# Performance work log

Measured on AMD Instinct MI355X. Metric: run time of the kernel, lower is better.

## Reference

```python
import jax, jax.numpy as jnp
import numpy as np

EMBED_DIM = 768
NUM_HEADS = 12
HEAD_DIM = EMBED_DIM // NUM_HEADS
SCALE = HEAD_DIM ** -0.5
LN_EPS = 1e-5


def layer_norm(x, gamma, beta):
    mu = jnp.mean(x, axis=-1, keepdims=True)
    var = jnp.var(x, axis=-1, keepdims=True)
    return (x - mu) * jax.lax.rsqrt(var + LN_EPS) * gamma + beta


def setup_inputs() -> dict:
    key = jax.random.key(0)
    ks = jax.random.split(key, 10)
    B, N, M, C = 4, 4096, 256, EMBED_DIM
    inp = {
        "input_tokens": jax.random.normal(ks[0], (B, N, C), dtype=jnp.float32),
        "query_tokens": jax.random.normal(ks[1], (B, M, C), dtype=jnp.float32),
        "Wq": jax.random.normal(ks[2], (C, C), dtype=jnp.float32) * 0.02,
        "bq": jnp.zeros((C,), dtype=jnp.float32),
        "Wk": jax.random.normal(ks[3], (C, C), dtype=jnp.float32) * 0.02,
        "bk": jnp.zeros((C,), dtype=jnp.float32),
        "Wv": jax.random.normal(ks[4], (C, C), dtype=jnp.float32) * 0.02,
        "bv": jnp.zeros((C,), dtype=jnp.float32),
        "gq_ln": jnp.ones((C,), dtype=jnp.float32),
        "bq_ln": jnp.zeros((C,), dtype=jnp.float32),
        "gk_ln": jnp.ones((C,), dtype=jnp.float32),
        "bk_ln": jnp.zeros((C,), dtype=jnp.float32),
    }
    return inp


def reference(input_tokens, query_tokens, Wq, bq, Wk, bk, Wv, bv,
              gq_ln, bq_ln, gk_ln, bk_ln):
    B, N, C = input_tokens.shape
    _, M, _ = query_tokens.shape
    H, D = NUM_HEADS, HEAD_DIM

    # v: Linear only (no LayerNorm on the attn=None path)
    v = (input_tokens @ Wv.T + bv).reshape(B, N, H, D).transpose(0, 2, 1, 3)   # [B,H,N,D]
    # q, k: Linear -> LayerNorm over full embed_dim, then split heads
    q = layer_norm(query_tokens @ Wq.T + bq, gq_ln, bq_ln)
    q = q.reshape(B, M, H, D).transpose(0, 2, 1, 3) * SCALE                    # [B,H,M,D]
    k = layer_norm(input_tokens @ Wk.T + bk, gk_ln, bk_ln)
    k = k.reshape(B, N, H, D).transpose(0, 2, 1, 3)                            # [B,H,N,D]

    attn = jax.nn.softmax(jnp.einsum('bhmd,bhnd->bhmn', q, k), axis=-1)        # [B,H,M,N]
    out = jnp.einsum('bhmn,bhnd->bhmd', attn, v)                               # [B,H,M,D]
    out = out.transpose(0, 2, 1, 3).reshape(B, M, C)
    return (query_tokens + out, attn)
```

## Files before the change

kernel.cpp:

```cpp
#include <hip/hip_runtime.h>
#include <math.h>

#define BB 4
#define NN 4096
#define MM 256
#define CC 768
#define HH 12
#define DD 64
#define SCALEF 0.125f
#define LN_EPSF 1e-5f

typedef __attribute__((ext_vector_type(4))) float f32x4;
typedef __attribute__((ext_vector_type(16))) float f32x16;
typedef __attribute__((ext_vector_type(8))) _Float16 f16x8;
typedef __attribute__((ext_vector_type(4))) _Float16 f16x4;

__device__ __forceinline__ void gldh(const _Float16* g, _Float16* l) {
    __builtin_amdgcn_global_load_lds(
        (const __attribute__((address_space(1))) void*)g,
        (__attribute__((address_space(3))) void*)l, 16, 0, 0);
}

__global__ __launch_bounds__(256) void conv_all(
    const float* __restrict__ x0, _Float16* __restrict__ y0, long long n0,
    const float* __restrict__ x1, _Float16* __restrict__ y1, long long n1,
    const float* __restrict__ x2, _Float16* __restrict__ y2, long long n2,
    const float* __restrict__ x3, _Float16* __restrict__ y3, long long n3,
    const float* __restrict__ x4, _Float16* __restrict__ y4, long long n4)
{
    long long i = ((long long)blockIdx.x * 256 + threadIdx.x) * 8;
    const long long total = n0 + n1 + n2 + n3 + n4;
    const long long stride = (long long)gridDim.x * 256 * 8;
    for (; i < total; i += stride) {
        const float* x; _Float16* y; long long off = i;
        if (off < n0) { x = x0; y = y0; }
        else if ((off -= n0) < n1) { x = x1; y = y1; }
        else if ((off -= n1) < n2) { x = x2; y = y2; }
        else if ((off -= n2) < n3) { x = x3; y = y3; }
        else { off -= n3; x = x4; y = y4; }
        float4 a = *(const float4*)(x + off);
        float4 b = *(const float4*)(x + off + 4);
        f16x8 o;
        o[0] = (_Float16)a.x; o[1] = (_Float16)a.y;
        o[2] = (_Float16)a.z; o[3] = (_Float16)a.w;
        o[4] = (_Float16)b.x; o[5] = (_Float16)b.y;
        o[6] = (_Float16)b.z; o[7] = (_Float16)b.w;
        *(f16x8*)(y + off) = o;
    }
}

__global__ __launch_bounds__(256) void proj_kv_f16(
    const _Float16* __restrict__ Xh,
    const _Float16* __restrict__ X2h,
    const _Float16* __restrict__ Wkh, const _Float16* __restrict__ Wqh,
    const _Float16* __restrict__ Wvh,
    const float* __restrict__ bk, const float* __restrict__ bq,
    const float* __restrict__ bv,
    _Float16* __restrict__ Klin, _Float16* __restrict__ Qlin,
    _Float16* __restrict__ Vth)
{
    __shared__ _Float16 As[2][4096];
    __shared__ _Float16 Bks[2][4096];
    __shared__ _Float16 Bvs[2][4096];

    const int bid = blockIdx.x;
    const _Float16* Ag; const _Float16* Bkg;
    const float* biask; _Float16* outk;
    bool hasV;
    int bm, bn;
    if (bid < 768) {
        bm = bid & 127; bn = bid >> 7;
        Ag = Xh; Bkg = Wkh; biask = bk; outk = Klin; hasV = true;
    } else {
        const int sid = bid - 768;
        bm = sid & 7; bn = sid >> 3;
        Ag = X2h; Bkg = Wqh; biask = bq; outk = Qlin; hasV = false;
    }
    const int row0 = bm * 128, col0 = bn * 128;

    const int tid = threadIdx.x;
    const int w = tid >> 6, lane = tid & 63;
    const int wr = w >> 1, wc = w & 1;
    const int fr = lane & 15, kg = lane >> 4;

    f32x4 acck[4][4], accv[4][4];
#pragma unroll
    for (int m = 0; m < 4; ++m)
#pragma unroll
        for (int n = 0; n < 4; ++n) {
            acck[m][n] = (f32x4){0.f, 0.f, 0.f, 0.f};
            accv[m][n] = (f32x4){0.f, 0.f, 0.f, 0.f};
        }

#define STAGE(sel, kt)                                                           \
    do {                                                                         \
        const int kk = (kt) << 5;                                                \
        _Pragma("unroll")                                                        \
        for (int i = 0; i < 2; ++i) {                                            \
            const int cbase = (i * 4 + w) * 64;                                  \
            const int c = cbase + lane;                                          \
            const int row = c >> 2, ks = (c & 3) << 3;                           \
            gldh(Ag  + (size_t)(row0 + row) * CC + kk + ks, &As[sel][cbase * 8]);\
            gldh(Bkg + (size_t)(col0 + row) * CC + kk + ks, &Bks[sel][cbase * 8]);\
            gldh(Wvh + (size_t)(col0 + row) * CC + kk + ks, &Bvs[sel][cbase * 8]);\
        }                                                                        \
    } while (0)

    STAGE(0, 0);
    int cur = 0;
    const int nk = CC >> 5;
    for (int kt = 0; kt < nk; ++kt) {
        __syncthreads();
        if (kt + 1 < nk) STAGE(cur ^ 1, kt + 1);
        const _Float16* lA = As[cur];
        const _Float16* lBk = Bks[cur];
        const _Float16* lBv = Bvs[cur];
        f16x8 a[4];
#pragma unroll
        for (int m = 0; m < 4; ++m)
            a[m] = *(const f16x8*)(lA + (wr * 64 + m * 16 + fr) * 32 + kg * 8);
#pragma unroll
        for (int n = 0; n < 4; ++n) {
            f16x8 bkf = *(const f16x8*)(lBk + (wc * 64 + n * 16 + fr) * 32 + kg * 8);
            __builtin_amdgcn_s_setprio(1);
#pragma unroll
            for (int m = 0; m < 4; ++m)
                acck[m][n] = __builtin_amdgcn_mfma_f32_16x16x32_f16(
                    a[m], bkf, acck[m][n], 0, 0, 0);
            __builtin_amdgcn_s_setprio(0);
            f16x8 bvf = *(const f16x8*)(lBv + (wc * 64 + n * 16 + fr) * 32 + kg * 8);
            __builtin_amdgcn_s_setprio(1);
#pragma unroll
            for (int m = 0; m < 4; ++m)
                accv[m][n] = __builtin_amdgcn_mfma_f32_16x16x32_f16(
                    a[m], bvf, accv[m][n], 0, 0, 0);
            __builtin_amdgcn_s_setprio(0);
        }
        cur ^= 1;
    }
#undef STAGE

    {
        float bvv[4];
#pragma unroll
        for (int n = 0; n < 4; ++n)
            bvv[n] = biask[col0 + wc * 64 + n * 16 + fr];
#pragma unroll
        for (int m = 0; m < 4; ++m)
#pragma unroll
            for (int n = 0; n < 4; ++n) {
                const int col = col0 + wc * 64 + n * 16 + fr;
#pragma unroll
                for (int r = 0; r < 4; ++r) {
                    const int row = row0 + wr * 64 + m * 16 + kg * 4 + r;
                    outk[(size_t)row * CC + col] = (_Float16)(acck[m][n][r] + bvv[n]);
                }
            }
    }
    if (hasV) {
        const int b = row0 >> 12;
        const int rb = row0 & 4095;
#pragma unroll
        for (int n = 0; n < 4; ++n) {
            const int cg = col0 + wc * 64 + n * 16 + fr;
            const int hh = cg >> 6, d = cg & 63;
            const float bb = bv[cg];
            _Float16* vrow = Vth + ((size_t)((b * HH + hh) * DD + d)) * NN + rb + wr * 64;
#pragma unroll
            for (int m = 0; m < 4; ++m) {
                f16x4 v4;
#pragma unroll
                for (int r = 0; r < 4; ++r)
                    v4[r] = (_Float16)(accv[m][n][r] + bb);
                *(f16x4*)(vrow + m * 16 + kg * 4) = v4;
            }
        }
    }
}

__global__ __launch_bounds__(256) void ln_rows_f16(
    const _Float16* __restrict__ Y, _Float16* __restrict__ outh,
    const float* __restrict__ g, const float* __restrict__ be, const float scale)
{
    const int row = blockIdx.x;
    const _Float16* y = Y + (size_t)row * CC;
    const int tid = threadIdx.x;
    float x0 = (float)y[tid], x1 = (float)y[tid + 256], x2 = (float)y[tid + 512];
    float s = x0 + x1 + x2;
    float q = x0 * x0 + x1 * x1 + x2 * x2;
#pragma unroll
    for (int o = 32; o >= 1; o >>= 1) {
        s += __shfl_xor(s, o, 64);
        q += __shfl_xor(q, o, 64);
    }
    __shared__ float sh_s[4], sh_q[4];
    const int w = tid >> 6;
    if ((tid & 63) == 0) { sh_s[w] = s; sh_q[w] = q; }
    __syncthreads();
    s = sh_s[0] + sh_s[1] + sh_s[2] + sh_s[3];
    q = sh_q[0] + sh_q[1] + sh_q[2] + sh_q[3];
    const float mu  = s * (1.f / 768.f);
    const float var = q * (1.f / 768.f) - mu * mu;
    const float inv = rsqrtf(var + LN_EPSF);
    _Float16* o = outh + (size_t)row * CC;
    o[tid]       = (_Float16)(((x0 - mu) * inv * g[tid]       + be[tid])       * scale);
    o[tid + 256] = (_Float16)(((x1 - mu) * inv * g[tid + 256] + be[tid + 256]) * scale);
    o[tid + 512] = (_Float16)(((x2 - mu) * inv * g[tid + 512] + be[tid + 512]) * scale);
}

__global__ __launch_bounds__(256, 4) void attn_stats(
    const _Float16* __restrict__ Qh,
    const _Float16* __restrict__ Kh,
    float* __restrict__ stats)
{
    __shared__ __align__(16) unsigned char smem[37888];
    _Float16* Kl = (_Float16*)smem;
    _Float16* Ql = (_Float16*)(smem + 32768);
    float (*red)[32][2] = (float(*)[32][2])(smem + 36864);

    const int tid = threadIdx.x;
    const int w = tid >> 6, lane = tid & 63;
    const int l5 = lane >> 5, lm = lane & 31;
    const int bid = blockIdx.x;
    const int mt = bid / 192;
    const int rem = bid % 192;
    const int bh = rem >> 2, ns = rem & 3;
    const int h = bh % HH, b = bh / HH;
    const int qr0 = mt * 32;
    const int nb = ns * 1024;

#define STAGEK(sel, c0)                                                         \
    _Pragma("unroll")                                                           \
    for (int i = 0; i < 4; ++i) {                                               \
        const int L = i * 256 + tid;                                            \
        const int n = L >> 3, pos = L & 7;                                      \
        gldh(Kh + (size_t)(b * NN + (c0) + n) * CC + h * DD + ((pos ^ (n & 7)) << 3), \
             &Kl[(sel) * 8192 + (i * 256 + w * 64) * 8]);                       \
    }

    {
        const int n = tid >> 3, pos = tid & 7;
        gldh(Qh + (size_t)(b * MM + qr0 + n) * CC + h * DD + ((pos ^ (n & 7)) << 3),
             &Ql[(w * 64) * 8]);
    }
    STAGEK(0, nb);
    __syncthreads();
    f16x8 qf[4];
#pragma unroll
    for (int ks = 0; ks < 4; ++ks)
        qf[ks] = *(const f16x8*)&Ql[lm * 64 + (((ks * 2 + l5) ^ (lm & 7)) << 3)];

    const int nl = w * 32 + lm;

    float mrun = -1e30f, srun = 0.f;
    int cur = 0;
    for (int c = 0; c < 8; ++c) {
        if (c) __syncthreads();
        if (c + 1 < 8) STAGEK(cur ^ 1, nb + (c + 1) * 128);
        const _Float16* Kb = Kl + cur * 8192;
        f32x16 s;
#pragma unroll
        for (int r = 0; r < 16; ++r) s[r] = 0.f;
        __builtin_amdgcn_s_setprio(1);
#pragma unroll
        for (int ks = 0; ks < 4; ++ks) {
            f16x8 kf = *(const f16x8*)&Kb[nl * 64 + (((ks * 2 + l5) ^ (nl & 7)) << 3)];
            s = __builtin_amdgcn_mfma_f32_32x32x16_f16(kf, qf[ks], s, 0, 0, 0);
        }
        __builtin_amdgcn_s_setprio(0);
        float cmax = s[0];
#pragma unroll
        for (int r = 1; r < 16; ++r) cmax = fmaxf(cmax, s[r]);
        cmax = fmaxf(cmax, __shfl_xor(cmax, 32, 64));
        const float nm = fmaxf(mrun, cmax);
        float cs = 0.f;
#pragma unroll
        for (int r = 0; r < 16; ++r) cs += __expf(s[r] - nm);
        cs += __shfl_xor(cs, 32, 64);
        srun = srun * __expf(mrun - nm) + cs;
        mrun = nm;
        cur ^= 1;
    }
    if (lane < 32) { red[w][lane][0] = mrun; red[w][lane][1] = srun; }
    __syncthreads();
    if (w == 0 && lane < 32) {
        float M = -1e30f;
#pragma unroll
        for (int ww = 0; ww < 4; ++ww) M = fmaxf(M, red[ww][lane][0]);
        float S = 0.f;
#pragma unroll
        for (int ww = 0; ww < 4; ++ww) S += red[ww][lane][1] * __expf(red[ww][lane][0] - M);
        float* sp = stats + ((size_t)((bh * 8 + mt) * 32 + lane)) * 8 + ns * 2;
        sp[0] = M; sp[1] = S;
    }
#undef STAGEK
}

__global__ __launch_bounds__(256, 2) void attn_main(
    const _Float16* __restrict__ Qh, const _Float16* __restrict__ Kh,
    const _Float16* __restrict__ Vt,
    const float* __restrict__ stats, const float* __restrict__ qtok,
    float* __restrict__ attn, float* __restrict__ out0)
{
    __shared__ __align__(16) unsigned char smem[77824];
    _Float16* Kl = (_Float16*)smem;
    _Float16* Vl = (_Float16*)(smem + 32768);
    _Float16* Ql = (_Float16*)(smem + 65536);
    _Float16* Pl = (_Float16*)(smem + 69632);
    float* rbuf = (float*)smem;

    const int tid = threadIdx.x;
    const int w = tid >> 6, lane = tid & 63;
    const int l5 = lane >> 5, lm = lane & 31;
    const int bh = blockIdx.x % 48;
    const int mt = blockIdx.x / 48;
    const int h = bh % HH, b = bh / HH;
    const int qr0 = mt * 32;

#define STAGEK(sel, c0)                                                         \
    _Pragma("unroll")                                                           \
    for (int i = 0; i < 4; ++i) {                                               \
        const int L = i * 256 + tid;                                            \
        const int n = L >> 3, pos = L & 7;                                      \
        gldh(Kh + (size_t)(b * NN + (c0) + n) * CC + h * DD + ((pos ^ (n & 7)) << 3), \
             &Kl[(sel) * 8192 + (i * 256 + w * 64) * 8]);                       \
    }
#define STAGEV(sel, c0)                                                         \
    _Pragma("unroll")                                                           \
    for (int i = 0; i < 4; ++i) {                                               \
        const int L = i * 256 + tid;                                            \
        const int d = L >> 4, pos = L & 15;                                     \
        const int blk = (pos & 8) | ((pos & 7) ^ (d & 7));                      \
        gldh(Vt + (size_t)(bh * DD + d) * NN + (c0) + blk * 8,                  \
             &Vl[(sel) * 8192 + (i * 256 + w * 64) * 8]);                       \
    }

    float M, invS;
    {
        const float* sp = stats + ((size_t)((bh * 8 + mt) * 32 + lm)) * 8;
        M = -1e30f;
#pragma unroll
        for (int n2 = 0; n2 < 4; ++n2) M = fmaxf(M, sp[n2 * 2]);
        float S = 0.f;
#pragma unroll
        for (int n2 = 0; n2 < 4; ++n2) S += sp[n2 * 2 + 1] * __expf(sp[n2 * 2] - M);
        invS = 1.f / S;
    }

    {
        const int n = tid >> 3, pos = tid & 7;
        gldh(Qh + (size_t)(b * MM + qr0 + n) * CC + h * DD + ((pos ^ (n & 7)) << 3),
             &Ql[(w * 64) * 8]);
    }
    STAGEK(0, 0); STAGEV(0, 0);
    __syncthreads();
    f16x8 qf[4];
#pragma unroll
    for (int ks = 0; ks < 4; ++ks)
        qf[ks] = *(const f16x8*)&Ql[lm * 64 + (((ks * 2 + l5) ^ (lm & 7)) << 3)];

    const int nl = w * 32 + lm;

    f32x16 oacc[2];
#pragma unroll
    for (int dt = 0; dt < 2; ++dt)
#pragma unroll
        for (int r = 0; r < 16; ++r) oacc[dt][r] = 0.f;

    float* attnRow = attn + ((size_t)(bh * MM + qr0 + lm)) * NN;

    int cur = 0;
    for (int c = 0; c < 32; ++c) {
        if (c) {
            asm volatile("s_waitcnt vmcnt(4)" ::: "memory");
            __builtin_amdgcn_s_barrier();
            __builtin_amdgcn_sched_barrier(0);
        }
        if (c + 1 < 32) { STAGEK(cur ^ 1, (c + 1) * 128); STAGEV(cur ^ 1, (c + 1) * 128); }
        __builtin_amdgcn_sched_barrier(0);
        const _Float16* Kb = Kl + cur * 8192;
        const _Float16* Vb = Vl + cur * 8192;
        f32x16 s;
#pragma unroll
        for (int r = 0; r < 16; ++r) s[r] = 0.f;
        __builtin_amdgcn_s_setprio(1);
#pragma unroll
        for (int ks = 0; ks < 4; ++ks) {
            f16x8 kf = *(const f16x8*)&Kb[nl * 64 + (((ks * 2 + l5) ^ (nl & 7)) << 3)];
            s = __builtin_amdgcn_mfma_f32_32x32x16_f16(kf, qf[ks], s, 0, 0, 0);
        }
        __builtin_amdgcn_s_setprio(0);
#pragma unroll
        for (int q = 0; q < 4; ++q) {
            float4 pw;
            f16x4 ph;
#pragma unroll
            for (int r = 0; r < 4; ++r) {
                const float p = __expf(s[q * 4 + r] - M) * invS;
                ((float*)&pw)[r] = p;
                ph[r] = (_Float16)p;
            }
            *(float4*)(attnRow + c * 128 + w * 32 + q * 8 + l5 * 4) = pw;
            const int blk16 = w * 4 + q;
            const int pos = (blk16 & 8) | ((blk16 & 7) ^ (lm & 7));
            *(f16x4*)&Pl[lm * 128 + pos * 8 + l5 * 4] = ph;
        }
        __builtin_amdgcn_s_setprio(1);
#pragma unroll
        for (int ks = 0; ks < 2; ++ks) {
            const int blk16 = w * 4 + ks * 2 + l5;
            const int posP = (blk16 & 8) | ((blk16 & 7) ^ (lm & 7));
            f16x8 pf = *(const f16x8*)&Pl[lm * 128 + posP * 8];
#pragma unroll
            for (int dt = 0; dt < 2; ++dt) {
                const int d = dt * 32 + lm;
                const int posV = (blk16 & 8) | ((blk16 & 7) ^ (d & 7));
                f16x8 vf = *(const f16x8*)&Vb[d * 128 + posV * 8];
                oacc[dt] = __builtin_amdgcn_mfma_f32_32x32x16_f16(pf, vf, oacc[dt], 0, 0, 0);
            }
        }
        __builtin_amdgcn_s_setprio(0);
        cur ^= 1;
    }

    __syncthreads();
#pragma unroll
    for (int dt = 0; dt < 2; ++dt)
#pragma unroll
        for (int r = 0; r < 16; ++r) {
            const int mrow = (r & 3) + 8 * (r >> 2) + 4 * l5;
            rbuf[w * 2048 + mrow * 64 + dt * 32 + lm] = oacc[dt][r];
        }
    __syncthreads();
    {
        const int m = tid >> 3, d0 = (tid & 7) * 8;
        const size_t obase = (size_t)(b * MM + qr0 + m) * CC + h * DD + d0;
#pragma unroll
        for (int j = 0; j < 8; ++j) {
            const int idx = m * 64 + d0 + j;
            float v = rbuf[idx] + rbuf[2048 + idx] + rbuf[4096 + idx] + rbuf[6144 + idx];
            out0[obase + j] = v + qtok[obase + j];
        }
    }
#undef STAGEK
#undef STAGEV
}

extern "C" void kernel_launch(void* const* d_in, const int* in_sizes, int n_in,
                              void* d_out, int out_size, void* d_ws, size_t ws_size,
                              hipStream_t stream) {
    (void)in_sizes; (void)n_in; (void)out_size; (void)ws_size;
    const float* input_tokens = (const float*)d_in[0];
    const float* query_tokens = (const float*)d_in[1];
    const float* Wq   = (const float*)d_in[2];
    const float* bq   = (const float*)d_in[3];
    const float* Wk   = (const float*)d_in[4];
    const float* bk   = (const float*)d_in[5];
    const float* Wv   = (const float*)d_in[6];
    const float* bv   = (const float*)d_in[7];
    const float* gq   = (const float*)d_in[8];
    const float* bqln = (const float*)d_in[9];
    const float* gk   = (const float*)d_in[10];
    const float* bkln = (const float*)d_in[11];

    float* out0 = (float*)d_out;
    float* attn = out0 + (size_t)BB * MM * CC;

    _Float16* hptr = (_Float16*)d_ws;
    _Float16* Klin = hptr;
    _Float16* Qlin = Klin + (size_t)BB * NN * CC;
    _Float16* Xh   = Qlin + (size_t)BB * MM * CC;
    _Float16* X2h  = Xh   + (size_t)BB * NN * CC;
    _Float16* Wkh  = X2h  + (size_t)BB * MM * CC;
    _Float16* Wqh  = Wkh  + (size_t)CC * CC;
    _Float16* Wvh  = Wqh  + (size_t)CC * CC;
    _Float16* Kh   = Wvh  + (size_t)CC * CC;
    _Float16* Qh   = Kh   + (size_t)BB * NN * CC;
    _Float16* Vt   = Qh   + (size_t)BB * MM * CC;
    float* stats   = (float*)(Vt + (size_t)BB * HH * DD * NN);

    conv_all<<<2048, 256, 0, stream>>>(
        input_tokens, Xh, (long long)BB * NN * CC,
        query_tokens, X2h, (long long)BB * MM * CC,
        Wk, Wkh, (long long)CC * CC,
        Wq, Wqh, (long long)CC * CC,
        Wv, Wvh, (long long)CC * CC);

    proj_kv_f16<<<816, 256, 0, stream>>>(Xh, X2h, Wkh, Wqh, Wvh,
                                         bk, bq, bv, Klin, Qlin, Vt);

    ln_rows_f16<<<BB * NN, 256, 0, stream>>>(Klin, Kh, gk, bkln, 1.0f);
    ln_rows_f16<<<BB * MM, 256, 0, stream>>>(Qlin, Qh, gq, bqln, SCALEF);

    attn_stats<<<1536, 256, 0, stream>>>(Qh, Kh, stats);
    attn_main<<<384, 256, 0, stream>>>(Qh, Kh, Vt, stats, query_tokens, attn, out0);
}
```

Before: 210.4 us.

## Reorder stats block mapping, use nontemporal attn stores, vectorize output epilogue

```diff
diff --git a/kernel.cpp b/kernel.cpp
--- a/kernel.cpp
+++ b/kernel.cpp
@@ -222,9 +222,9 @@
     const int w = tid >> 6, lane = tid & 63;
     const int l5 = lane >> 5, lm = lane & 31;
     const int bid = blockIdx.x;
-    const int mt = bid / 192;
-    const int rem = bid % 192;
-    const int bh = rem >> 2, ns = rem & 3;
+    const int bh = bid % 48;
+    const int t  = bid / 48;
+    const int mt = t >> 2, ns = t & 3;
     const int h = bh % HH, b = bh / HH;
     const int qr0 = mt * 32;
     const int nb = ns * 1024;
@@ -371,13 +371,8 @@
 
     int cur = 0;
     for (int c = 0; c < 32; ++c) {
-        if (c) {
-            asm volatile("s_waitcnt vmcnt(4)" ::: "memory");
-            __builtin_amdgcn_s_barrier();
-            __builtin_amdgcn_sched_barrier(0);
-        }
+        if (c) __syncthreads();
         if (c + 1 < 32) { STAGEK(cur ^ 1, (c + 1) * 128); STAGEV(cur ^ 1, (c + 1) * 128); }
-        __builtin_amdgcn_sched_barrier(0);
         const _Float16* Kb = Kl + cur * 8192;
         const _Float16* Vb = Vl + cur * 8192;
         f32x16 s;
@@ -392,15 +387,16 @@
         __builtin_amdgcn_s_setprio(0);
 #pragma unroll
         for (int q = 0; q < 4; ++q) {
-            float4 pw;
+            f32x4 pw;
             f16x4 ph;
 #pragma unroll
             for (int r = 0; r < 4; ++r) {
                 const float p = __expf(s[q * 4 + r] - M) * invS;
-                ((float*)&pw)[r] = p;
+                pw[r] = p;
                 ph[r] = (_Float16)p;
             }
-            *(float4*)(attnRow + c * 128 + w * 32 + q * 8 + l5 * 4) = pw;
+            __builtin_nontemporal_store(
+                pw, (f32x4*)(attnRow + c * 128 + w * 32 + q * 8 + l5 * 4));
             const int blk16 = w * 4 + q;
             const int pos = (blk16 & 8) | ((blk16 & 7) ^ (lm & 7));
             *(f16x4*)&Pl[lm * 128 + pos * 8 + l5 * 4] = ph;
@@ -435,12 +431,23 @@
     {
         const int m = tid >> 3, d0 = (tid & 7) * 8;
         const size_t obase = (size_t)(b * MM + qr0 + m) * CC + h * DD + d0;
-#pragma unroll
-        for (int j = 0; j < 8; ++j) {
+        f32x4 v0, v1;
+#pragma unroll
+        for (int j = 0; j < 4; ++j) {
             const int idx = m * 64 + d0 + j;
-            float v = rbuf[idx] + rbuf[2048 + idx] + rbuf[4096 + idx] + rbuf[6144 + idx];
-            out0[obase + j] = v + qtok[obase + j];
-        }
+            v0[j] = rbuf[idx] + rbuf[2048 + idx] + rbuf[4096 + idx] + rbuf[6144 + idx];
+        }
+#pragma unroll
+        for (int j = 0; j < 4; ++j) {
+            const int idx = m * 64 + d0 + 4 + j;
+            v1[j] = rbuf[idx] + rbuf[2048 + idx] + rbuf[4096 + idx] + rbuf[6144 + idx];
+        }
+        float4 q0 = *(const float4*)(qtok + obase);
+        float4 q1 = *(const float4*)(qtok + obase + 4);
+        v0[0] += q0.x; v0[1] += q0.y; v0[2] += q0.z; v0[3] += q0.w;
+        v1[0] += q1.x; v1[1] += q1.y; v1[2] += q1.z; v1[3] += q1.w;
+        __builtin_nontemporal_store(v0, (f32x4*)(out0 + obase));
+        __builtin_nontemporal_store(v1, (f32x4*)(out0 + obase + 4));
     }
 #undef STAGEK
 #undef STAGEV
```

Result: slower. 404.4 us (+92.2%).
